# Optimization experiments

Hardware: AMD Instinct MI355X
Metric: run time of the kernel (lower is better)

Reference implementation:

```python
import jax, jax.numpy as jnp
import numpy as np

N_HEAD = 16
ROPE_BASE = 10000.0
EPS = 1e-6


def _rms_norm(x):
    return x / jnp.sqrt(jnp.mean(x * x, axis=-1, keepdims=True) + EPS)


def _rotary_cos_sin(n_pos, dim, dtype):
    # NOTE: faithful to the source, n_pos == n_head (not seq_len) because
    # Rotary.forward reads x.shape[2] of a (B,T,H,D) tensor.
    inv_freq = 1.0 / (ROPE_BASE ** (jnp.arange(0, dim, 2, dtype=jnp.float32) / dim))
    t = jnp.arange(n_pos, dtype=jnp.float32)
    freqs = jnp.outer(t, inv_freq)  # (n_pos, dim//2)
    return jnp.cos(freqs).astype(dtype)[None, None], jnp.sin(freqs).astype(dtype)[None, None]


def _apply_rotary(x, cos, sin):
    d = x.shape[-1] // 2
    x1, x2 = x[..., :d], x[..., d:]
    return jnp.concatenate([x1 * cos + x2 * sin, -x1 * sin + x2 * cos], axis=-1)


def setup_inputs() -> dict:
    key = jax.random.key(0)
    ks = jax.random.split(key, 8)
    B, T, C = 4, 1024, 2048
    x = jax.random.normal(ks[0], (B, T, C), dtype=jnp.float32)
    v1 = jax.random.normal(ks[1], (B, T, N_HEAD, C // N_HEAD), dtype=jnp.float32)
    s = 0.02
    W_qkv = jax.random.normal(ks[2], (C, 3 * C), dtype=jnp.float32) * s
    b_qkv = jax.random.normal(ks[3], (3 * C,), dtype=jnp.float32) * s
    W_proj = jax.random.normal(ks[4], (C, C), dtype=jnp.float32) * s
    b_proj = jax.random.normal(ks[5], (C,), dtype=jnp.float32) * s
    lamb = jnp.float32(0.5)
    return {"x": x, "v1": v1, "W_qkv": W_qkv, "b_qkv": b_qkv,
            "W_proj": W_proj, "b_proj": b_proj, "lamb": lamb}


def reference(x, v1, W_qkv, b_qkv, W_proj, b_proj, lamb):
    B, T, C = x.shape
    H = N_HEAD
    D = C // H
    qkv = x @ W_qkv + b_qkv  # (B,T,3C)
    q, k, v = jnp.split(qkv, 3, axis=-1)
    q = q.reshape(B, T, H, D)
    k = k.reshape(B, T, H, D)
    v = v.reshape(B, T, H, D)
    v1 = v1.reshape(B, T, H, D)
    value = (1.0 - lamb) * v + lamb * v1  # lambda value-residual mix
    q = _rms_norm(q)
    k = _rms_norm(k)
    cos, sin = _rotary_cos_sin(H, D, x.dtype)  # rotary over head axis (source bug, kept)
    q = _apply_rotary(q, cos, sin)
    k = _apply_rotary(k, cos, sin)
    # causal attention, default flex_attention scale 1/sqrt(D)
    scale = 1.0 / jnp.sqrt(jnp.float32(D)).astype(x.dtype)
    scores = jnp.einsum('bqhd,bkhd->bhqk', q, k) * scale
    causal = jnp.tril(jnp.ones((T, T), dtype=bool))
    scores = jnp.where(causal[None, None], scores, jnp.finfo(scores.dtype).min)
    probs = jax.nn.softmax(scores, axis=-1)
    attn = jnp.einsum('bhqk,bkhd->bqhd', probs, value).reshape(B, T, C)
    out = attn @ W_proj + b_proj
    return out, v1
```

## Files before the change

kernel.cpp:

```cpp
#include <hip/hip_runtime.h>
#include <stdint.h>
#include <stddef.h>

typedef unsigned short u16;
typedef __attribute__((ext_vector_type(8))) short  bf16x8;
typedef __attribute__((ext_vector_type(4))) unsigned short u16x4;
typedef __attribute__((ext_vector_type(4))) float  f32x4;

#define DEVI __device__ __forceinline__

DEVI float bf2f(u16 u){ union{uint32_t i; float f;} v; v.i = ((uint32_t)u)<<16; return v.f; }
DEVI u16 f2bf(float f){ union{float f; uint32_t i;} v; v.f=f; uint32_t r = v.i + 0x7fffu + ((v.i>>16)&1u); return (u16)(r>>16); }

DEVI void gload_lds16(const void* g, void* l){
  __builtin_amdgcn_global_load_lds((const __attribute__((address_space(1))) void*)g,
                                   (__attribute__((address_space(3))) void*)l, 16, 0, 0);
}

__global__ void k_cvt_bf16(const float* __restrict__ in, u16* __restrict__ out, int n){
  int i = (blockIdx.x*256 + threadIdx.x)*4;
  int st = gridDim.x*256*4;
  for (; i < n; i += st){
    f32x4 v = *(const f32x4*)(in + i);
    u16x4 o;
    #pragma unroll
    for (int j=0;j<4;j++) o[j] = f2bf(v[j]);
    *(u16x4*)(out + i) = o;
  }
}

__global__ __launch_bounds__(256) void k_transpose_cvt(const float* __restrict__ in, u16* __restrict__ out, int K, int N){
  __shared__ float tile[32][33];
  int nb = blockIdx.x*32, kb = blockIdx.y*32;
  int tx = threadIdx.x & 31, ty = threadIdx.x >> 5;
  #pragma unroll
  for (int i=0;i<32;i+=8)
    tile[ty+i][tx] = in[(size_t)(kb+ty+i)*N + nb+tx];
  __syncthreads();
  #pragma unroll
  for (int i=0;i<32;i+=8)
    out[(size_t)(nb+ty+i)*K + kb+tx] = f2bf(tile[tx][ty+i]);
}

template<bool OUT_BF16>
__global__ __launch_bounds__(256) void k_gemm_bt(
    const u16* __restrict__ A, const u16* __restrict__ Bt,
    const float* __restrict__ bias, void* __restrict__ Cout,
    int M, int N, int K, int nbn)
{
  __shared__ __attribute__((aligned(16))) u16 sA[128*64];
  __shared__ __attribute__((aligned(16))) u16 sB[128*64];
  int nwg = gridDim.x;
  int orig = blockIdx.x;
  int wgid = (orig & 7)*(nwg>>3) + (orig>>3);
  int bm = wgid / nbn, bn = wgid % nbn;
  const int tid = threadIdx.x;
  const int w = tid>>6, l = tid&63;
  const int lr = l&15, lg = l>>4;
  const int wr = (w>>1)*64, wc = (w&1)*64;
  const size_t rowA = (size_t)bm*128;
  const size_t rowB = (size_t)bn*128;
  f32x4 acc[4][4] = {};
  for (int k0=0; k0<K; k0+=64){
    #pragma unroll
    for (int it=0; it<4; ++it){
      int c = it*256 + tid;
      int r = c>>3, k8 = (c&7) ^ (r&7);
      gload_lds16(A + (rowA+r)*K + k0 + k8*8, &sA[c*8]);
    }
    #pragma unroll
    for (int it=0; it<4; ++it){
      int c = it*256 + tid;
      int r = c>>3, k8 = (c&7) ^ (r&7);
      gload_lds16(Bt + (rowB+r)*K + k0 + k8*8, &sB[c*8]);
    }
    __syncthreads();
    #pragma unroll
    for (int ks=0; ks<2; ++ks){
      bf16x8 af[4], bfr[4];
      #pragma unroll
      for (int m=0;m<4;m++){
        int row = wr + m*16 + lr, k = ks*32 + lg*8;
        int byt = ((row<<7) + (k<<1)) ^ ((row&7)<<4);
        af[m] = *(const bf16x8*)((const char*)sA + byt);
      }
      #pragma unroll
      for (int n=0;n<4;n++){
        int row = wc + n*16 + lr, k = ks*32 + lg*8;
        int byt = ((row<<7) + (k<<1)) ^ ((row&7)<<4);
        bfr[n] = *(const bf16x8*)((const char*)sB + byt);
      }
      #pragma unroll
      for (int m=0;m<4;m++)
        #pragma unroll
        for (int n=0;n<4;n++)
          acc[m][n] = __builtin_amdgcn_mfma_f32_16x16x32_bf16(af[m], bfr[n], acc[m][n], 0,0,0);
    }
    __syncthreads();
  }
  #pragma unroll
  for (int n=0;n<4;n++){
    int col = bn*128 + wc + n*16 + lr;
    float bv = bias[col];
    #pragma unroll
    for (int m=0;m<4;m++){
      #pragma unroll
      for (int j=0;j<4;j++){
        int row = bm*128 + wr + m*16 + lg*4 + j;
        float v = acc[m][n][j] + bv;
        if (OUT_BF16) ((u16*)Cout)[(size_t)row*N + col] = f2bf(v);
        else          ((float*)Cout)[(size_t)row*N + col] = v;
      }
    }
  }
}

DEVI void unpack16(const u16* p, float* f){
  bf16x8 a = *(const bf16x8*)p, b = *(const bf16x8*)(p+8);
  #pragma unroll
  for (int i=0;i<8;i++){ f[i]=bf2f((u16)a[i]); f[8+i]=bf2f((u16)b[i]); }
}

__global__ __launch_bounds__(256) void k_qkv_post(
    const u16*  __restrict__ qkv,
    const float* __restrict__ v1,
    const float* __restrict__ lambp,
    u16* __restrict__ qn,
    u16* __restrict__ kn,
    u16* __restrict__ vT)
{
  __shared__ float cosv[64], sinv[64];
  __shared__ __attribute__((aligned(16))) u16 sv[64][136];
  int bid = blockIdx.x;
  int tb = bid & 15, h = (bid>>4)&15, b = bid>>8;
  int tid = threadIdx.x;
  if (tid < 64){
    float ang = (float)h * exp2f(-(float)tid * 0.2076205059304595f);
    cosv[tid] = cosf(ang);
    sinv[tid] = sinf(ang);
  }
  float lamb = lambp[0];
  int row = tid>>2, p = tid&3;
  int t = tb*64 + row;
  size_t base = ((size_t)(b*1024 + t))*6144 + (size_t)h*128;
  __syncthreads();

  #pragma unroll
  for (int qc=0; qc<2; ++qc){
    const u16* src = qkv + base + qc*2048;
    u16* dst = (qc==0 ? qn : kn) + ((size_t)(b*1024+t))*2048 + h*128;
    int j0 = p*16;
    float x1[16], x2[16];
    unpack16(src + j0, x1);
    unpack16(src + 64 + j0, x2);
    float ss = 0.f;
    #pragma unroll
    for (int i=0;i<16;i++) ss += x1[i]*x1[i] + x2[i]*x2[i];
    ss += __shfl_xor(ss, 1);
    ss += __shfl_xor(ss, 2);
    float rn = rsqrtf(ss*(1.0f/128.0f) + 1e-6f);
    bf16x8 o1a,o1b,o2a,o2b;
    #pragma unroll
    for (int i=0;i<16;i++){
      float c = cosv[j0+i], s = sinv[j0+i];
      u16 a = f2bf(( x1[i]*c + x2[i]*s)*rn);
      u16 bq= f2bf((-x1[i]*s + x2[i]*c)*rn);
      if (i<8){ o1a[i]=(short)a; o2a[i]=(short)bq; } else { o1b[i-8]=(short)a; o2b[i-8]=(short)bq; }
    }
    *(bf16x8*)(dst + j0)      = o1a;
    *(bf16x8*)(dst + j0 + 8)  = o1b;
    *(bf16x8*)(dst + 64 + j0)     = o2a;
    *(bf16x8*)(dst + 64 + j0 + 8) = o2b;
  }

  {
    const u16* srcv = qkv + base + 4096;
    const float* src1 = v1 + (((size_t)(b*1024+t))*16 + h)*128;
    int d0 = p*32;
    #pragma unroll
    for (int c8=0;c8<4;c8++){
      bf16x8 vv = *(const bf16x8*)(srcv + d0 + c8*8);
      f32x4 a0 = *(const f32x4*)(src1 + d0 + c8*8);
      f32x4 a1 = *(const f32x4*)(src1 + d0 + c8*8 + 4);
      bf16x8 o;
      #pragma unroll
      for (int i=0;i<8;i++){
        float x1v = (i<4)? a0[i] : a1[i-4];
        o[i] = (short)f2bf((1.0f-lamb)*bf2f((u16)vv[i]) + lamb*x1v);
      }
      *(bf16x8*)(&sv[row][d0 + c8*8]) = o;
    }
  }
  __syncthreads();
  {
    int d = tid>>1, tc = (tid&1)*32;
    u16 tmp[32];
    #pragma unroll
    for (int i=0;i<32;i++) tmp[i] = sv[tc+i][d];
    u16* dst = vT + (((size_t)(b*16+h))*128 + d)*1024 + tb*64 + tc;
    #pragma unroll
    for (int c8=0;c8<4;c8++){
      bf16x8 o;
      #pragma unroll
      for (int i=0;i<8;i++) o[i]=(short)tmp[c8*8+i];
      *(bf16x8*)(dst + c8*8) = o;
    }
  }
}

__global__ __launch_bounds__(256) void k_attn(
    const u16* __restrict__ Q,
    const u16* __restrict__ Kn,
    const u16* __restrict__ Vt,
    u16* __restrict__ O)
{
  __shared__ __attribute__((aligned(16))) u16 sK[2][64*128];
  __shared__ __attribute__((aligned(16))) u16 sV[2][128*64];
  __shared__ __attribute__((aligned(16))) u16 sP[4][16*64];
  int bid = blockIdx.x;
  int qi = 15 - (bid>>6);
  int bh = bid & 63;
  int h = bh & 15, b = bh >> 4;
  int tid = threadIdx.x, w = tid>>6, l = tid&63, lr = l&15, lg = l>>4;
  int qrow = qi*64 + w*16;
  bf16x8 aq[4];
  {
    const u16* qp = Q + ((size_t)(b*1024 + qrow + lr))*2048 + h*128 + lg*8;
    #pragma unroll
    for (int ks=0; ks<4; ++ks) aq[ks] = *(const bf16x8*)(qp + ks*32);
  }
  f32x4 accO[8] = {};
  float mrun[4], srun[4];
  #pragma unroll
  for (int j=0;j<4;j++){ mrun[j] = -INFINITY; srun[j]=0.f; }
  const float scale = 0.08838834764831845f;
  const size_t kbase = (size_t)(b*1024)*2048 + (size_t)h*128;
  const u16* vbase = Vt + ((size_t)(b*16+h))*128*1024;

  auto STAGE = [&](int kt, int buf){
    #pragma unroll
    for (int it=0; it<4; ++it){
      int c = it*256+tid;
      int key = c>>4, d16 = (c&15)^(key&7);
      gload_lds16(Kn + kbase + (size_t)(kt*64+key)*2048 + d16*8, &sK[buf][c*8]);
    }
    #pragma unroll
    for (int it=0; it<4; ++it){
      int c = it*256+tid;
      int d = c>>3, k8 = (c&7)^(d&7);
      gload_lds16(vbase + (size_t)d*1024 + kt*64 + k8*8, &sV[buf][c*8]);
    }
  };

  STAGE(0, 0);
  int cur = 0;
  for (int kt=0; kt<=qi; ++kt){
    if (kt < qi){
      STAGE(kt+1, cur^1);
      asm volatile("s_waitcnt vmcnt(8)" ::: "memory");
    } else {
      asm volatile("s_waitcnt vmcnt(0)" ::: "memory");
    }
    __builtin_amdgcn_s_barrier();
    __builtin_amdgcn_sched_barrier(0);
    const char* kb = (const char*)sK[cur];
    const char* vb = (const char*)sV[cur];

    f32x4 accS[4] = {};
    __builtin_amdgcn_s_setprio(1);
    #pragma unroll
    for (int ks=0; ks<4; ++ks){
      #pragma unroll
      for (int n=0;n<4;n++){
        int key = n*16+lr, k = ks*32+lg*8;
        int byt = ((key<<8) + (k<<1)) ^ ((key&7)<<4);
        bf16x8 bk = *(const bf16x8*)(kb + byt);
        accS[n] = __builtin_amdgcn_mfma_f32_16x16x32_bf16(aq[ks], bk, accS[n], 0,0,0);
      }
    }
    __builtin_amdgcn_s_setprio(0);
    bool diag = (kt == qi);
    float pj[4][4];
    #pragma unroll
    for (int j=0;j<4;j++){
      int qg = qrow + lg*4 + j;
      float mx = -INFINITY;
      #pragma unroll
      for (int n=0;n<4;n++){
        float s = accS[n][j]*scale;
        if (diag && (kt*64 + n*16 + lr) > qg) s = -1e30f;
        pj[n][j] = s;
        mx = fmaxf(mx, s);
      }
      #pragma unroll
      for (int off=1; off<16; off<<=1) mx = fmaxf(mx, __shfl_xor(mx, off));
      float mnew = fmaxf(mrun[j], mx);
      float fac = __expf(mrun[j] - mnew);
      float ps = 0.f;
      #pragma unroll
      for (int n=0;n<4;n++){ float e = __expf(pj[n][j]-mnew); pj[n][j]=e; ps += e; }
      #pragma unroll
      for (int off=1; off<16; off<<=1) ps += __shfl_xor(ps, off);
      srun[j] = srun[j]*fac + ps;
      mrun[j] = mnew;
      #pragma unroll
      for (int n=0;n<8;n++) accO[n][j] *= fac;
    }
    #pragma unroll
    for (int n=0;n<4;n++)
      #pragma unroll
      for (int j=0;j<4;j++){
        int q = lg*4+j, key = n*16+lr;
        int byt = ((q<<7) + (key<<1)) ^ ((q&7)<<4);
        *(u16*)((char*)sP[w] + byt) = f2bf(pj[n][j]);
      }
    bf16x8 pA[2];
    #pragma unroll
    for (int ks=0; ks<2; ++ks){
      int k = ks*32 + lg*8;
      int byt = ((lr<<7) + (k<<1)) ^ ((lr&7)<<4);
      pA[ks] = *(const bf16x8*)((const char*)sP[w] + byt);
    }
    __builtin_amdgcn_s_setprio(1);
    #pragma unroll
    for (int ks=0; ks<2; ++ks)
      #pragma unroll
      for (int n=0;n<8;n++){
        int d = n*16+lr, k = ks*32+lg*8;
        int byt = ((d<<7) + (k<<1)) ^ ((d&7)<<4);
        bf16x8 bv = *(const bf16x8*)(vb + byt);
        accO[n] = __builtin_amdgcn_mfma_f32_16x16x32_bf16(pA[ks], bv, accO[n], 0,0,0);
      }
    __builtin_amdgcn_s_setprio(0);
    __builtin_amdgcn_s_barrier();
    cur ^= 1;
  }
  #pragma unroll
  for (int j=0;j<4;j++){
    float inv = 1.0f / srun[j];
    int row = qrow + lg*4 + j;
    u16* op = O + ((size_t)(b*1024+row))*2048 + h*128;
    #pragma unroll
    for (int n=0;n<8;n++)
      op[n*16+lr] = f2bf(accO[n][j]*inv);
  }
}

extern "C" void kernel_launch(void* const* d_in, const int* in_sizes, int n_in,
                              void* d_out, int out_size, void* d_ws, size_t ws_size,
                              hipStream_t stream)
{
  const float* x     = (const float*)d_in[0];
  const float* v1    = (const float*)d_in[1];
  const float* Wqkv  = (const float*)d_in[2];
  const float* bqkv  = (const float*)d_in[3];
  const float* Wproj = (const float*)d_in[4];
  const float* bproj = (const float*)d_in[5];
  const float* lamb  = (const float*)d_in[6];

  char* ws = (char*)d_ws;
  u16* qkv_b  = (u16*)(ws);
  u16* WqkvT  = (u16*)(ws +  50331648);
  u16* WprojT = (u16*)(ws +  75497472);
  u16* xb     = (u16*)(ws +  83886080);
  u16* vT     = xb;
  u16* qn     = (u16*)(ws + 100663296);
  u16* kn     = (u16*)(ws + 117440512);
  u16* attn_b = qkv_b;

  float* out = (float*)d_out;

  hipLaunchKernelGGL(k_cvt_bf16, dim3(2048), dim3(256), 0, stream, x, xb, 8388608);
  hipLaunchKernelGGL(k_transpose_cvt, dim3(192, 64), dim3(256), 0, stream, Wqkv,  WqkvT,  2048, 6144);
  hipLaunchKernelGGL(k_transpose_cvt, dim3(64, 64),  dim3(256), 0, stream, Wproj, WprojT, 2048, 2048);
  hipLaunchKernelGGL((k_gemm_bt<true>),  dim3(32*48), dim3(256), 0, stream, xb, WqkvT, bqkv, (void*)qkv_b, 4096, 6144, 2048, 48);
  hipLaunchKernelGGL(k_qkv_post, dim3(1024), dim3(256), 0, stream, qkv_b, v1, lamb, qn, kn, vT);
  hipLaunchKernelGGL(k_attn, dim3(1024), dim3(256), 0, stream, qn, kn, vT, attn_b);
  hipLaunchKernelGGL((k_gemm_bt<false>), dim3(32*16), dim3(256), 0, stream, attn_b, WprojT, bproj, (void*)out, 4096, 2048, 2048, 16);
  hipMemcpyAsync(out + 8388608, v1, 8388608*sizeof(float), hipMemcpyDeviceToDevice, stream);
}
```

Measured before the change: 289.8 us.

## Add 256x256 pipelined GEMM for QKV and fuse v1 passthrough copy

Adds a new 512-thread GEMM kernel with 256x256 tiles, double-buffered LDS loaded asynchronously via global_load_lds, a swizzled LDS layout, and interleaved MFMA/load scheduling with barriers. It replaces the 128-tile QKV projection GEMM, aiming for more data reuse and better overlap of memory and compute. It also removes the separate device-to-device memcpy of v1 to the output by writing v1 from inside the qkv post-processing kernel, which already reads it. Risks include register pressure from the large accumulator, lower occupancy, and fewer workgroups (384) than CUs times waves can easily balance.

```diff
diff --git a/kernel.cpp b/kernel.cpp
--- a/kernel.cpp
+++ b/kernel.cpp
@@ -40,6 +40,149 @@
   #pragma unroll
   for (int i=0;i<32;i+=8)
     out[(size_t)(nb+ty+i)*K + kb+tx] = f2bf(tile[tx][ty+i]);
+}
+
+#define STG(LP, GP, KH) \
+  gload_lds16((GP) + offs[0] + (KH)*32, (LP) + (KH)*8192 + tid*8); \
+  gload_lds16((GP) + offs[1] + (KH)*32, (LP) + (KH)*8192 + 4096 + tid*8);
+
+#define RD_A(SP, KH, MH, DST) \
+  { _Pragma("unroll") for (int f=0; f<4; f++){ \
+      int row_ = wm*128 + (MH)*64 + f*16 + lr; \
+      int rp_ = row_>>1; \
+      int slot_ = ((((row_&1)<<2) | lg) ^ (rp_&7)); \
+      DST[f] = *(const bf16x8*)((const char*)(SP) + (KH)*16384 + rp_*128 + slot_*16); } }
+
+#define RD_B(SP, KH, DST) \
+  { _Pragma("unroll") for (int nf=0; nf<4; nf++){ \
+      int row_ = wn*64 + nf*16 + lr; \
+      int rp_ = row_>>1; \
+      int slot_ = ((((row_&1)<<2) | lg) ^ (rp_&7)); \
+      DST[nf] = *(const bf16x8*)((const char*)(SP) + (KH)*16384 + rp_*128 + slot_*16); } }
+
+#define MMQ(MH, AA, BB) \
+  __builtin_amdgcn_s_setprio(1); \
+  { _Pragma("unroll") for (int f=0; f<4; f++) \
+    { _Pragma("unroll") for (int nf=0; nf<4; nf++) \
+      acc[(MH)*4+f][nf] = __builtin_amdgcn_mfma_f32_16x16x32_bf16(AA[f], BB[nf], acc[(MH)*4+f][nf], 0,0,0); } } \
+  __builtin_amdgcn_s_setprio(0);
+
+#define BAR_LGKM \
+  __builtin_amdgcn_s_barrier(); \
+  __builtin_amdgcn_sched_barrier(0); \
+  asm volatile("s_waitcnt lgkmcnt(0)" ::: "memory"); \
+  __builtin_amdgcn_sched_barrier(0);
+
+#define WAITV(N) asm volatile("s_waitcnt vmcnt(" #N ")" ::: "memory");
+#define ORDER_FENCE __builtin_amdgcn_sched_barrier(0); asm volatile("" ::: "memory");
+
+template<bool OUT_BF16>
+__global__ __launch_bounds__(512) void k_gemm256(
+    const u16* __restrict__ A, const u16* __restrict__ Bt,
+    const float* __restrict__ bias, void* __restrict__ Cout,
+    int M, int N, int K, int nbn)
+{
+  __shared__ __attribute__((aligned(16))) u16 sAm[2][2][8192];
+  __shared__ __attribute__((aligned(16))) u16 sBm[2][2][8192];
+  int nwg = gridDim.x;
+  int orig = blockIdx.x;
+  int wgid = (orig & 7)*(nwg>>3) + (orig>>3);
+  int bm = wgid / nbn, bn = wgid % nbn;
+  const int tid = threadIdx.x;
+  const int wid = tid>>6, l = tid&63;
+  const int lr = l&15, lg = l>>4;
+  const int wm = wid>>2, wn = wid&3;
+  const size_t rowA = (size_t)bm*256;
+  const size_t rowB = (size_t)bn*256;
+
+  uint32_t offs[2];
+  #pragma unroll
+  for (int it=0; it<2; it++){
+    int cc = it*512 + tid;
+    int rp = cc>>3, comb = (cc&7) ^ (rp&7);
+    int row = rp*2 + (comb>>2), k16 = comb&3;
+    offs[it] = (uint32_t)(row*K + k16*8);
+  }
+  const u16* Abase = A + rowA*K;
+  const u16* Bbase = Bt + rowB*K;
+
+  f32x4 acc[8][4] = {};
+  bf16x8 a0[4], a1[4], b0[4], b1[4];
+  const int NT = K>>6;
+
+  STG(&sAm[0][0][0], Abase, 0);
+  STG(&sBm[0][0][0], Bbase, 0);
+  ORDER_FENCE;
+  STG(&sAm[0][0][0], Abase, 1);
+  STG(&sBm[0][0][0], Bbase, 1);
+  WAITV(0);
+  __builtin_amdgcn_s_barrier();
+  __builtin_amdgcn_sched_barrier(0);
+
+  const u16* An = Abase + 64;
+  const u16* Bn = Bbase + 64;
+  for (int kt=0; kt<NT-1; ++kt){
+    const u16* sAr = &sAm[kt&1][0][0];
+    const u16* sBr = &sBm[kt&1][0][0];
+    u16* sAw = &sAm[(kt&1)^1][0][0];
+    u16* sBw = &sBm[(kt&1)^1][0][0];
+    RD_B(sBr, 0, b0);
+    RD_A(sAr, 0, 0, a0);
+    STG(sAw, An, 0);
+    BAR_LGKM;
+    MMQ(0, a0, b0);
+    RD_A(sAr, 0, 1, a1);
+    STG(sBw, Bn, 0);
+    WAITV(4);
+    BAR_LGKM;
+    MMQ(1, a1, b0);
+    RD_B(sBr, 1, b1);
+    RD_A(sAr, 1, 0, a0);
+    STG(sAw, An, 1);
+    BAR_LGKM;
+    MMQ(0, a0, b1);
+    RD_A(sAr, 1, 1, a1);
+    STG(sBw, Bn, 1);
+    WAITV(4);
+    BAR_LGKM;
+    MMQ(1, a1, b1);
+    An += 64; Bn += 64;
+  }
+  {
+    const u16* sAr = &sAm[(NT-1)&1][0][0];
+    const u16* sBr = &sBm[(NT-1)&1][0][0];
+    RD_B(sBr, 0, b0);
+    RD_A(sAr, 0, 0, a0);
+    BAR_LGKM;
+    MMQ(0, a0, b0);
+    RD_A(sAr, 0, 1, a1);
+    WAITV(0);
+    BAR_LGKM;
+    MMQ(1, a1, b0);
+    RD_B(sBr, 1, b1);
+    RD_A(sAr, 1, 0, a0);
+    BAR_LGKM;
+    MMQ(0, a0, b1);
+    RD_A(sAr, 1, 1, a1);
+    BAR_LGKM;
+    MMQ(1, a1, b1);
+  }
+
+  #pragma unroll
+  for (int nf=0; nf<4; nf++){
+    int col = bn*256 + wn*64 + nf*16 + lr;
+    float bv = bias[col];
+    #pragma unroll
+    for (int m=0; m<8; m++){
+      #pragma unroll
+      for (int j=0; j<4; j++){
+        int row = bm*256 + wm*128 + m*16 + lg*4 + j;
+        float v = acc[m][nf][j] + bv;
+        if (OUT_BF16) ((u16*)Cout)[(size_t)row*N + col] = f2bf(v);
+        else          ((float*)Cout)[(size_t)row*N + col] = v;
+      }
+    }
+  }
 }
 
 template<bool OUT_BF16>
@@ -127,7 +270,8 @@
     const float* __restrict__ lambp,
     u16* __restrict__ qn,
     u16* __restrict__ kn,
-    u16* __restrict__ vT)
+    u16* __restrict__ vT,
+    float* __restrict__ v1out)
 {
   __shared__ float cosv[64], sinv[64];
   __shared__ __attribute__((aligned(16))) u16 sv[64][136];
@@ -175,13 +319,17 @@
 
   {
     const u16* srcv = qkv + base + 4096;
-    const float* src1 = v1 + (((size_t)(b*1024+t))*16 + h)*128;
+    size_t v1off = (((size_t)(b*1024+t))*16 + h)*128;
+    const float* src1 = v1 + v1off;
+    float* dst1 = v1out + v1off;
     int d0 = p*32;
     #pragma unroll
     for (int c8=0;c8<4;c8++){
       bf16x8 vv = *(const bf16x8*)(srcv + d0 + c8*8);
       f32x4 a0 = *(const f32x4*)(src1 + d0 + c8*8);
       f32x4 a1 = *(const f32x4*)(src1 + d0 + c8*8 + 4);
+      *(f32x4*)(dst1 + d0 + c8*8) = a0;
+      *(f32x4*)(dst1 + d0 + c8*8 + 4) = a1;
       bf16x8 o;
       #pragma unroll
       for (int i=0;i<8;i++){
@@ -373,9 +521,8 @@
   hipLaunchKernelGGL(k_cvt_bf16, dim3(2048), dim3(256), 0, stream, x, xb, 8388608);
   hipLaunchKernelGGL(k_transpose_cvt, dim3(192, 64), dim3(256), 0, stream, Wqkv,  WqkvT,  2048, 6144);
   hipLaunchKernelGGL(k_transpose_cvt, dim3(64, 64),  dim3(256), 0, stream, Wproj, WprojT, 2048, 2048);
-  hipLaunchKernelGGL((k_gemm_bt<true>),  dim3(32*48), dim3(256), 0, stream, xb, WqkvT, bqkv, (void*)qkv_b, 4096, 6144, 2048, 48);
-  hipLaunchKernelGGL(k_qkv_post, dim3(1024), dim3(256), 0, stream, qkv_b, v1, lamb, qn, kn, vT);
+  hipLaunchKernelGGL((k_gemm256<true>), dim3(384), dim3(512), 0, stream, xb, WqkvT, bqkv, (void*)qkv_b, 4096, 6144, 2048, 24);
+  hipLaunchKernelGGL(k_qkv_post, dim3(1024), dim3(256), 0, stream, qkv_b, v1, lamb, qn, kn, vT, out + 8388608);
   hipLaunchKernelGGL(k_attn, dim3(1024), dim3(256), 0, stream, qn, kn, vT, attn_b);
   hipLaunchKernelGGL((k_gemm_bt<false>), dim3(32*16), dim3(256), 0, stream, attn_b, WprojT, bproj, (void*)out, 4096, 2048, 2048, 16);
-  hipMemcpyAsync(out + 8388608, v1, 8388608*sizeof(float), hipMemcpyDeviceToDevice, stream);
-}
+}
```

Result: no change. 289.6 us (-0.1%).

## Use triple-buffered 128x256 GEMM and fuse v1 passthrough copy into qkv_post

Applied to the files above, without the earlier changes.

Replaces the 128x128 single-buffered GEMM with a 512-thread 128x256 tile kernel. It uses a three-stage LDS ring of half-K slabs, explicit vmcnt/lgkmcnt waits, barriers and MFMA priority hints, so global-to-LDS loads overlap with matrix math. Separately, the device-to-device memcpy of v1 into the output is removed, and k_qkv_post writes v1 to the output while it already reads it. The new schedule depends on hand-tuned wait counts, and the projection GEMM now launches only 256 workgroups, which may underfill the GPU.

```diff
diff --git a/kernel.cpp b/kernel.cpp
--- a/kernel.cpp
+++ b/kernel.cpp
@@ -42,72 +42,112 @@
     out[(size_t)(nb+ty+i)*K + kb+tx] = f2bf(tile[tx][ty+i]);
 }
 
+#define STG_A(SLAB, GSRC) \
+  gload_lds16((GSRC) + off0, (SLAB) + tid*8);
+#define STG_B(SLAB, GSRC) \
+  gload_lds16((GSRC) + off0, (SLAB) + tid*8); \
+  gload_lds16((GSRC) + off1, (SLAB) + 4096 + tid*8);
+
+#define RD4(SLAB, ROWBASE, DST) \
+  { _Pragma("unroll") for (int f=0; f<4; f++){ \
+      int row_ = (ROWBASE) + f*16 + lr; \
+      int rp_ = row_>>1; \
+      int slot_ = ((((row_&1)<<2) | lg) ^ (rp_&7)); \
+      DST[f] = *(const bf16x8*)((const char*)(SLAB) + rp_*128 + slot_*16); } }
+
+#define MM16(AA, BB) \
+  __builtin_amdgcn_s_setprio(1); \
+  { _Pragma("unroll") for (int f=0; f<4; f++) \
+    { _Pragma("unroll") for (int nf=0; nf<4; nf++) \
+      acc[f][nf] = __builtin_amdgcn_mfma_f32_16x16x32_bf16(AA[f], BB[nf], acc[f][nf], 0,0,0); } } \
+  __builtin_amdgcn_s_setprio(0);
+
+#define BAR_LGKM \
+  __builtin_amdgcn_s_barrier(); \
+  __builtin_amdgcn_sched_barrier(0); \
+  asm volatile("s_waitcnt lgkmcnt(0)" ::: "memory"); \
+  __builtin_amdgcn_sched_barrier(0);
+
+#define WAITV(N) asm volatile("s_waitcnt vmcnt(" #N ")" ::: "memory");
+#define ORDER_FENCE __builtin_amdgcn_sched_barrier(0); asm volatile("" ::: "memory");
+
 template<bool OUT_BF16>
-__global__ __launch_bounds__(256) void k_gemm_bt(
+__global__ __launch_bounds__(512) void k_gemm128x256(
     const u16* __restrict__ A, const u16* __restrict__ Bt,
     const float* __restrict__ bias, void* __restrict__ Cout,
     int M, int N, int K, int nbn)
 {
-  __shared__ __attribute__((aligned(16))) u16 sA[128*64];
-  __shared__ __attribute__((aligned(16))) u16 sB[128*64];
+  __shared__ __attribute__((aligned(16))) u16 sA[3][2][4096];
+  __shared__ __attribute__((aligned(16))) u16 sB[3][2][8192];
   int nwg = gridDim.x;
   int orig = blockIdx.x;
   int wgid = (orig & 7)*(nwg>>3) + (orig>>3);
   int bm = wgid / nbn, bn = wgid % nbn;
   const int tid = threadIdx.x;
-  const int w = tid>>6, l = tid&63;
+  const int wid = tid>>6, l = tid&63;
   const int lr = l&15, lg = l>>4;
-  const int wr = (w>>1)*64, wc = (w&1)*64;
-  const size_t rowA = (size_t)bm*128;
-  const size_t rowB = (size_t)bn*128;
+  const int wm = wid>>2, wn = wid&3;
+  const int rba = wm*64, rbb = wn*64;
+
+  uint32_t off0, off1;
+  { int cc=tid;     int rp=cc>>3, cb=(cc&7)^(rp&7); off0 = (uint32_t)((rp*2+(cb>>2))*K + (cb&3)*8); }
+  { int cc=512+tid; int rp=cc>>3, cb=(cc&7)^(rp&7); off1 = (uint32_t)((rp*2+(cb>>2))*K + (cb&3)*8); }
+  const u16* Ab = A + (size_t)bm*128*K;
+  const u16* Bb = Bt + (size_t)bn*256*K;
+
   f32x4 acc[4][4] = {};
-  for (int k0=0; k0<K; k0+=64){
-    #pragma unroll
-    for (int it=0; it<4; ++it){
-      int c = it*256 + tid;
-      int r = c>>3, k8 = (c&7) ^ (r&7);
-      gload_lds16(A + (rowA+r)*K + k0 + k8*8, &sA[c*8]);
-    }
-    #pragma unroll
-    for (int it=0; it<4; ++it){
-      int c = it*256 + tid;
-      int r = c>>3, k8 = (c&7) ^ (r&7);
-      gload_lds16(Bt + (rowB+r)*K + k0 + k8*8, &sB[c*8]);
-    }
-    __syncthreads();
-    #pragma unroll
-    for (int ks=0; ks<2; ++ks){
-      bf16x8 af[4], bfr[4];
-      #pragma unroll
-      for (int m=0;m<4;m++){
-        int row = wr + m*16 + lr, k = ks*32 + lg*8;
-        int byt = ((row<<7) + (k<<1)) ^ ((row&7)<<4);
-        af[m] = *(const bf16x8*)((const char*)sA + byt);
-      }
-      #pragma unroll
-      for (int n=0;n<4;n++){
-        int row = wc + n*16 + lr, k = ks*32 + lg*8;
-        int byt = ((row<<7) + (k<<1)) ^ ((row&7)<<4);
-        bfr[n] = *(const bf16x8*)((const char*)sB + byt);
-      }
-      #pragma unroll
-      for (int m=0;m<4;m++)
-        #pragma unroll
-        for (int n=0;n<4;n++)
-          acc[m][n] = __builtin_amdgcn_mfma_f32_16x16x32_bf16(af[m], bfr[n], acc[m][n], 0,0,0);
-    }
-    __syncthreads();
-  }
-  #pragma unroll
-  for (int n=0;n<4;n++){
-    int col = bn*128 + wc + n*16 + lr;
+  bf16x8 a0[4], a1[4], b0[4], b1[4];
+  const int NT = K>>6;
+
+  STG_B(&sB[0][0][0], Bb);      STG_A(&sA[0][0][0], Ab);      ORDER_FENCE;
+  STG_B(&sB[0][1][0], Bb+32);   STG_A(&sA[0][1][0], Ab+32);   ORDER_FENCE;
+  STG_B(&sB[1][0][0], Bb+64);   STG_A(&sA[1][0][0], Ab+64);
+  WAITV(6);
+  __builtin_amdgcn_s_barrier();
+  __builtin_amdgcn_sched_barrier(0);
+
+  int s0=0, s1=1, s2=2;
+  for (int t=0; t<=NT-3; ++t){
+    const u16* A1 = Ab + (t+1)*64;  const u16* B1 = Bb + (t+1)*64;
+    const u16* A2 = Ab + (t+2)*64;  const u16* B2 = Bb + (t+2)*64;
+    RD4(&sB[s0][0][0], rbb, b0); RD4(&sA[s0][0][0], rba, a0);
+    STG_B(&sB[s1][1][0], B1+32); STG_A(&sA[s1][1][0], A1+32);
+    WAITV(6);
+    BAR_LGKM; MM16(a0, b0);
+    RD4(&sB[s0][1][0], rbb, b1); RD4(&sA[s0][1][0], rba, a1);
+    STG_B(&sB[s2][0][0], B2);    STG_A(&sA[s2][0][0], A2);
+    WAITV(6);
+    BAR_LGKM; MM16(a1, b1);
+    int tmp=s0; s0=s1; s1=s2; s2=tmp;
+  }
+  {
+    const u16* A1 = Ab + (NT-1)*64;  const u16* B1 = Bb + (NT-1)*64;
+    RD4(&sB[s0][0][0], rbb, b0); RD4(&sA[s0][0][0], rba, a0);
+    STG_B(&sB[s1][1][0], B1+32); STG_A(&sA[s1][1][0], A1+32);
+    WAITV(6);
+    BAR_LGKM; MM16(a0, b0);
+    RD4(&sB[s0][1][0], rbb, b1); RD4(&sA[s0][1][0], rba, a1);
+    WAITV(3);
+    BAR_LGKM; MM16(a1, b1);
+  }
+  {
+    RD4(&sB[s1][0][0], rbb, b0); RD4(&sA[s1][0][0], rba, a0);
+    WAITV(0);
+    BAR_LGKM; MM16(a0, b0);
+    RD4(&sB[s1][1][0], rbb, b1); RD4(&sA[s1][1][0], rba, a1);
+    BAR_LGKM; MM16(a1, b1);
+  }
+
+  #pragma unroll
+  for (int nf=0; nf<4; nf++){
+    int col = bn*256 + wn*64 + nf*16 + lr;
     float bv = bias[col];
     #pragma unroll
-    for (int m=0;m<4;m++){
-      #pragma unroll
-      for (int j=0;j<4;j++){
-        int row = bm*128 + wr + m*16 + lg*4 + j;
-        float v = acc[m][n][j] + bv;
+    for (int m=0; m<4; m++){
+      #pragma unroll
+      for (int j=0; j<4; j++){
+        int row = bm*128 + wm*64 + m*16 + lg*4 + j;
+        float v = acc[m][nf][j] + bv;
         if (OUT_BF16) ((u16*)Cout)[(size_t)row*N + col] = f2bf(v);
         else          ((float*)Cout)[(size_t)row*N + col] = v;
       }
@@ -127,7 +167,8 @@
     const float* __restrict__ lambp,
     u16* __restrict__ qn,
     u16* __restrict__ kn,
-    u16* __restrict__ vT)
+    u16* __restrict__ vT,
+    float* __restrict__ v1out)
 {
   __shared__ float cosv[64], sinv[64];
   __shared__ __attribute__((aligned(16))) u16 sv[64][136];
@@ -175,13 +216,17 @@
 
   {
     const u16* srcv = qkv + base + 4096;
-    const float* src1 = v1 + (((size_t)(b*1024+t))*16 + h)*128;
+    size_t v1off = (((size_t)(b*1024+t))*16 + h)*128;
+    const float* src1 = v1 + v1off;
+    float* dst1 = v1out + v1off;
     int d0 = p*32;
     #pragma unroll
     for (int c8=0;c8<4;c8++){
       bf16x8 vv = *(const bf16x8*)(srcv + d0 + c8*8);
       f32x4 a0 = *(const f32x4*)(src1 + d0 + c8*8);
       f32x4 a1 = *(const f32x4*)(src1 + d0 + c8*8 + 4);
+      *(f32x4*)(dst1 + d0 + c8*8) = a0;
+      *(f32x4*)(dst1 + d0 + c8*8 + 4) = a1;
       bf16x8 o;
       #pragma unroll
       for (int i=0;i<8;i++){
@@ -373,9 +418,8 @@
   hipLaunchKernelGGL(k_cvt_bf16, dim3(2048), dim3(256), 0, stream, x, xb, 8388608);
   hipLaunchKernelGGL(k_transpose_cvt, dim3(192, 64), dim3(256), 0, stream, Wqkv,  WqkvT,  2048, 6144);
   hipLaunchKernelGGL(k_transpose_cvt, dim3(64, 64),  dim3(256), 0, stream, Wproj, WprojT, 2048, 2048);
-  hipLaunchKernelGGL((k_gemm_bt<true>),  dim3(32*48), dim3(256), 0, stream, xb, WqkvT, bqkv, (void*)qkv_b, 4096, 6144, 2048, 48);
-  hipLaunchKernelGGL(k_qkv_post, dim3(1024), dim3(256), 0, stream, qkv_b, v1, lamb, qn, kn, vT);
+  hipLaunchKernelGGL((k_gemm128x256<true>),  dim3(768), dim3(512), 0, stream, xb, WqkvT, bqkv, (void*)qkv_b, 4096, 6144, 2048, 24);
+  hipLaunchKernelGGL(k_qkv_post, dim3(1024), dim3(256), 0, stream, qkv_b, v1, lamb, qn, kn, vT, out + 8388608);
   hipLaunchKernelGGL(k_attn, dim3(1024), dim3(256), 0, stream, qn, kn, vT, attn_b);
-  hipLaunchKernelGGL((k_gemm_bt<false>), dim3(32*16), dim3(256), 0, stream, attn_b, WprojT, bproj, (void*)out, 4096, 2048, 2048, 16);
-  hipMemcpyAsync(out + 8388608, v1, 8388608*sizeof(float), hipMemcpyDeviceToDevice, stream);
-}
+  hipLaunchKernelGGL((k_gemm128x256<false>), dim3(256), dim3(512), 0, stream, attn_b, WprojT, bproj, (void*)out, 4096, 2048, 2048, 8);
+}
```

Result: faster. 280.7 us (-3.1%).
